# Kernel optimization log

Measured on AMD Instinct MI355X. Metric: run time of the kernel, lower is better.

## Reference

```python
import jax, jax.numpy as jnp
import numpy as np

N_NODES = 100000
N_EDGES = 1600000
IN_DIM, HID_DIM, LAT_DIM = 128, 128, 32


def gcn_conv(x, W, b, src, dst, ew, num_nodes):
    """PyG GCNConv with improved=True (self-loop fill value 2.0),
    symmetric normalization D^-1/2 (A + 2I) D^-1/2, then linear + bias."""
    loop = jnp.arange(num_nodes)
    src2 = jnp.concatenate([src, loop])
    dst2 = jnp.concatenate([dst, loop])
    ew2 = jnp.concatenate([ew, jnp.full((num_nodes,), 2.0, dtype=x.dtype)])
    # deg[i] = sum of incoming edge weights (incl. self loop weight 2)
    deg = jax.ops.segment_sum(ew2, dst2, num_segments=num_nodes)
    dinv = jnp.where(deg > 0, jax.lax.rsqrt(deg), 0.0)
    norm = dinv[src2] * ew2 * dinv[dst2]           # [E+N]
    h = x @ W                                      # linear first: [N, out]
    msg = h[src2] * norm[:, None]                  # gather + scale: [E+N, out]
    out = jax.ops.segment_sum(msg, dst2, num_segments=num_nodes)
    return out + b


def setup_inputs() -> dict:
    key = jax.random.key(0)
    ks = jax.random.split(key, 8)
    x = jax.random.normal(ks[0], (N_NODES, IN_DIM), dtype=jnp.float32)
    edge_index = jax.random.randint(ks[1], (2, N_EDGES), 0, N_NODES, dtype=jnp.int64)
    edge_weight = jnp.ones((N_EDGES,), dtype=jnp.float32)
    s = 1.0 / np.sqrt(IN_DIM)
    W1 = jax.random.normal(ks[2], (IN_DIM, HID_DIM), dtype=jnp.float32) * s
    b1 = jnp.zeros((HID_DIM,), dtype=jnp.float32)
    sh = 1.0 / np.sqrt(HID_DIM)
    Wm = jax.random.normal(ks[3], (HID_DIM, LAT_DIM), dtype=jnp.float32) * sh
    bm = jnp.zeros((LAT_DIM,), dtype=jnp.float32)
    Ws = jax.random.normal(ks[4], (HID_DIM, LAT_DIM), dtype=jnp.float32) * sh
    bs = jnp.zeros((LAT_DIM,), dtype=jnp.float32)
    return {"x": x, "edge_index": edge_index, "edge_weight": edge_weight,
            "W1": W1, "b1": b1, "Wm": Wm, "bm": bm, "Ws": Ws, "bs": bs}


def reference(x, edge_index, edge_weight, W1, b1, Wm, bm, Ws, bs):
    src, dst = edge_index[0], edge_index[1]
    n = x.shape[0]
    h = gcn_conv(x, W1, b1, src, dst, edge_weight, n)
    h = jax.nn.relu(h)
    z_mean = gcn_conv(h, Wm, bm, src, dst, edge_weight, n)
    z_logstd = gcn_conv(h, Ws, bs, src, dst, edge_weight, n)
    return (z_mean, z_logstd)
```

## Files before the change

### kernel.cpp

```cpp
#include <hip/hip_runtime.h>


#define DIM 128
#define LAT 32
#define SCAN_ELEMS 1024

typedef short bf16x8 __attribute__((ext_vector_type(8)));
typedef float f32x4 __attribute__((ext_vector_type(4)));

__device__ __forceinline__ unsigned short f2bf(float f) {
    unsigned u = __float_as_uint(f);
    return (unsigned short)((u + 0x7fffu + ((u >> 16) & 1u)) >> 16);
}
__device__ __forceinline__ unsigned packbf(float a, float b) {
    return (unsigned)f2bf(a) | ((unsigned)f2bf(b) << 16);
}
__device__ __forceinline__ float2 bfp2f(unsigned u) {
    float2 r;
    r.x = __uint_as_float(u << 16);
    r.y = __uint_as_float(u & 0xffff0000u);
    return r;
}

__global__ __launch_bounds__(256) void k_prep(const int* __restrict__ dst,
                                              int* __restrict__ cursor,
                                              unsigned short* __restrict__ rank, int E,
                                              const float* __restrict__ x,
                                              uint4* __restrict__ xb,
                                              const float* __restrict__ W1,
                                              const float* __restrict__ Wm,
                                              const float* __restrict__ Ws,
                                              unsigned short* __restrict__ w1t,
                                              unsigned short* __restrict__ wct,
                                              int RB, int XB) {
    const int b = blockIdx.x;
    if (b < RB) {
        int idx = b * 1024 + threadIdx.x * 4;
        if (idx + 3 < E) {
            int4 d4 = *reinterpret_cast<const int4*>(dst + idx);
            unsigned short r0 = (unsigned short)atomicAdd(&cursor[d4.x], 1);
            unsigned short r1 = (unsigned short)atomicAdd(&cursor[d4.y], 1);
            unsigned short r2 = (unsigned short)atomicAdd(&cursor[d4.z], 1);
            unsigned short r3 = (unsigned short)atomicAdd(&cursor[d4.w], 1);
            ushort4 r = {r0, r1, r2, r3};
            *reinterpret_cast<ushort4*>(rank + idx) = r;
        } else {
            for (int j = 0; j < 4 && idx + j < E; ++j)
                rank[idx + j] = (unsigned short)atomicAdd(&cursor[dst[idx + j]], 1);
        }
    } else if (b < RB + XB) {
        size_t i = ((size_t)(b - RB) * 256 + threadIdx.x) * 16;
        const float4* xin = reinterpret_cast<const float4*>(x + i);
        float4 v0 = xin[0], v1 = xin[1], v2 = xin[2], v3 = xin[3];
        uint4 o0, o1;
        o0.x = packbf(v0.x, v0.y); o0.y = packbf(v0.z, v0.w);
        o0.z = packbf(v1.x, v1.y); o0.w = packbf(v1.z, v1.w);
        o1.x = packbf(v2.x, v2.y); o1.y = packbf(v2.z, v2.w);
        o1.z = packbf(v3.x, v3.y); o1.w = packbf(v3.z, v3.w);
        xb[i / 8] = o0;
        xb[i / 8 + 1] = o1;
    } else {
        int i = (b - RB - XB) * 256 + threadIdx.x;
        if (i < DIM * DIM) {
            int c = i >> 7, k = i & 127;
            w1t[c * DIM + k] = f2bf(W1[k * DIM + c]);
        }
        i -= DIM * DIM;
        if (i >= 0 && i < 64 * DIM) {
            int c = i >> 7, k = i & 127;
            wct[c * DIM + k] = f2bf((c < LAT) ? Wm[k * LAT + c] : Ws[k * LAT + (c - LAT)]);
        }
    }
}

__global__ __launch_bounds__(256) void k_scan1(const int* __restrict__ counts,
                                               int* __restrict__ rowptr,
                                               int* __restrict__ bsums, int N) {
    __shared__ int sdata[256];
    const int t = threadIdx.x;
    const int base = blockIdx.x * SCAN_ELEMS + t * 4;
    int v[4];
#pragma unroll
    for (int j = 0; j < 4; ++j) {
        int idx = base + j;
        v[j] = (idx < N) ? counts[idx] : 0;
    }
    int tot = v[0] + v[1] + v[2] + v[3];
    sdata[t] = tot;
    __syncthreads();
    for (int off = 1; off < 256; off <<= 1) {
        int x = 0;
        if (t >= off) x = sdata[t - off];
        __syncthreads();
        if (t >= off) sdata[t] += x;
        __syncthreads();
    }
    int running = sdata[t] - tot;
#pragma unroll
    for (int j = 0; j < 4; ++j) {
        int idx = base + j;
        if (idx < N) rowptr[idx] = running;
        running += v[j];
    }
    if (t == 255) bsums[blockIdx.x] = sdata[255];
}

__global__ __launch_bounds__(256) void k_scanfix(int* __restrict__ rowptr,
                                                 const int* __restrict__ bsums,
                                                 int N, int E) {
    __shared__ int pfx;
    if (threadIdx.x == 0) {
        int s = 0;
        for (int j = 0; j < (int)blockIdx.x; ++j) s += bsums[j];
        pfx = s;
        if (blockIdx.x == 0) rowptr[N] = E;
    }
    __syncthreads();
    int s = pfx;
    int base = blockIdx.x * SCAN_ELEMS + threadIdx.x * 4;
#pragma unroll
    for (int j = 0; j < 4; ++j) {
        int idx = base + j;
        if (idx < N) rowptr[idx] += s;
    }
}

__global__ void k_place(const int* __restrict__ src, const int* __restrict__ dst,
                        const float* __restrict__ ew, const unsigned short* __restrict__ rank,
                        const int* __restrict__ rowptr, int2* __restrict__ csr, int E) {
    int e = blockIdx.x * blockDim.x + threadIdx.x;
    if (e < E)
        csr[rowptr[dst[e]] + rank[e]] = make_int2(src[e], __float_as_int(ew[e]));
}

__global__ void k_degseg(const int2* __restrict__ csr, const int* __restrict__ rowptr,
                         float* __restrict__ dinv, int N) {
    int i = blockIdx.x * blockDim.x + threadIdx.x;
    if (i >= N) return;
    float deg = 2.0f;
    int p = rowptr[i], end = rowptr[i + 1];
    for (; p < end; ++p) deg += __int_as_float(csr[p].y);
    dinv[i] = (deg > 0.0f) ? rsqrtf(deg) : 0.0f;
}

__global__ __launch_bounds__(256) void k_gather128(const int2* __restrict__ csr,
                                                   const int* __restrict__ rowptr,
                                                   const float* __restrict__ dinv,
                                                   const uint4* __restrict__ xb,
                                                   uint4* __restrict__ axb, int N) {
    int node = (blockIdx.x * 256 + threadIdx.x) >> 6;
    int lane = threadIdx.x & 63;
    if (node >= N) return;
    const int q = lane >> 4;
    const int l = lane & 15;
    float di = dinv[node];
    float acc[8];
#pragma unroll
    for (int j = 0; j < 8; ++j) acc[j] = 0.f;
    if (q == 0) {
        uint4 sv = xb[(size_t)node * 16 + l];
        float sl = 2.0f * di;
        float2 s0 = bfp2f(sv.x), s1 = bfp2f(sv.y), s2 = bfp2f(sv.z), s3 = bfp2f(sv.w);
        acc[0] = s0.x * sl; acc[1] = s0.y * sl;
        acc[2] = s1.x * sl; acc[3] = s1.y * sl;
        acc[4] = s2.x * sl; acc[5] = s2.y * sl;
        acc[6] = s3.x * sl; acc[7] = s3.y * sl;
    }
    int p = rowptr[node] + q;
    int end = rowptr[node + 1];
    for (; p + 12 < end; p += 16) {
        int2 e0 = csr[p], e1 = csr[p + 4], e2 = csr[p + 8], e3 = csr[p + 12];
        float n0 = __int_as_float(e0.y) * dinv[e0.x];
        float n1 = __int_as_float(e1.y) * dinv[e1.x];
        float n2 = __int_as_float(e2.y) * dinv[e2.x];
        float n3 = __int_as_float(e3.y) * dinv[e3.x];
        uint4 u0 = xb[(size_t)e0.x * 16 + l];
        uint4 u1 = xb[(size_t)e1.x * 16 + l];
        uint4 u2 = xb[(size_t)e2.x * 16 + l];
        uint4 u3 = xb[(size_t)e3.x * 16 + l];
        {
            float2 a0 = bfp2f(u0.x), a1 = bfp2f(u0.y), a2 = bfp2f(u0.z), a3 = bfp2f(u0.w);
            acc[0] = fmaf(a0.x, n0, acc[0]); acc[1] = fmaf(a0.y, n0, acc[1]);
            acc[2] = fmaf(a1.x, n0, acc[2]); acc[3] = fmaf(a1.y, n0, acc[3]);
            acc[4] = fmaf(a2.x, n0, acc[4]); acc[5] = fmaf(a2.y, n0, acc[5]);
            acc[6] = fmaf(a3.x, n0, acc[6]); acc[7] = fmaf(a3.y, n0, acc[7]);
        }
        {
            float2 a0 = bfp2f(u1.x), a1 = bfp2f(u1.y), a2 = bfp2f(u1.z), a3 = bfp2f(u1.w);
            acc[0] = fmaf(a0.x, n1, acc[0]); acc[1] = fmaf(a0.y, n1, acc[1]);
            acc[2] = fmaf(a1.x, n1, acc[2]); acc[3] = fmaf(a1.y, n1, acc[3]);
            acc[4] = fmaf(a2.x, n1, acc[4]); acc[5] = fmaf(a2.y, n1, acc[5]);
            acc[6] = fmaf(a3.x, n1, acc[6]); acc[7] = fmaf(a3.y, n1, acc[7]);
        }
        {
            float2 a0 = bfp2f(u2.x), a1 = bfp2f(u2.y), a2 = bfp2f(u2.z), a3 = bfp2f(u2.w);
            acc[0] = fmaf(a0.x, n2, acc[0]); acc[1] = fmaf(a0.y, n2, acc[1]);
            acc[2] = fmaf(a1.x, n2, acc[2]); acc[3] = fmaf(a1.y, n2, acc[3]);
            acc[4] = fmaf(a2.x, n2, acc[4]); acc[5] = fmaf(a2.y, n2, acc[5]);
            acc[6] = fmaf(a3.x, n2, acc[6]); acc[7] = fmaf(a3.y, n2, acc[7]);
        }
        {
            float2 a0 = bfp2f(u3.x), a1 = bfp2f(u3.y), a2 = bfp2f(u3.z), a3 = bfp2f(u3.w);
            acc[0] = fmaf(a0.x, n3, acc[0]); acc[1] = fmaf(a0.y, n3, acc[1]);
            acc[2] = fmaf(a1.x, n3, acc[2]); acc[3] = fmaf(a1.y, n3, acc[3]);
            acc[4] = fmaf(a2.x, n3, acc[4]); acc[5] = fmaf(a2.y, n3, acc[5]);
            acc[6] = fmaf(a3.x, n3, acc[6]); acc[7] = fmaf(a3.y, n3, acc[7]);
        }
    }
    for (; p < end; p += 4) {
        int2 e0 = csr[p];
        float n0 = __int_as_float(e0.y) * dinv[e0.x];
        uint4 u0 = xb[(size_t)e0.x * 16 + l];
        float2 a0 = bfp2f(u0.x), a1 = bfp2f(u0.y), a2 = bfp2f(u0.z), a3 = bfp2f(u0.w);
        acc[0] = fmaf(a0.x, n0, acc[0]); acc[1] = fmaf(a0.y, n0, acc[1]);
        acc[2] = fmaf(a1.x, n0, acc[2]); acc[3] = fmaf(a1.y, n0, acc[3]);
        acc[4] = fmaf(a2.x, n0, acc[4]); acc[5] = fmaf(a2.y, n0, acc[5]);
        acc[6] = fmaf(a3.x, n0, acc[6]); acc[7] = fmaf(a3.y, n0, acc[7]);
    }
#pragma unroll
    for (int j = 0; j < 8; ++j) {
        acc[j] += __shfl_xor(acc[j], 16);
        acc[j] += __shfl_xor(acc[j], 32);
    }
    if (q == 0) {
        uint4 o;
        o.x = packbf(acc[0] * di, acc[1] * di);
        o.y = packbf(acc[2] * di, acc[3] * di);
        o.z = packbf(acc[4] * di, acc[5] * di);
        o.w = packbf(acc[6] * di, acc[7] * di);
        axb[(size_t)node * 16 + l] = o;
    }
}

__global__ __launch_bounds__(256) void k_mfma_mlp(const unsigned short* __restrict__ axb,
                                                  const unsigned short* __restrict__ w1t,
                                                  const unsigned short* __restrict__ wct,
                                                  const float* __restrict__ b1,
                                                  unsigned short* __restrict__ hwb, int N) {
    __shared__ __align__(16) unsigned short hs[4][16][136];
    const int wave = threadIdx.x >> 6;
    const int lane = threadIdx.x & 63;
    const int lrow = lane & 15;
    const int lk = lane >> 4;
    const int R0 = blockIdx.x * 64 + wave * 16;
    const bool active = (R0 < N);

    if (active) {
        f32x4 acc[8];
#pragma unroll
        for (int t = 0; t < 8; ++t) acc[t] = (f32x4){0.f, 0.f, 0.f, 0.f};
        const unsigned short* arow = axb + (size_t)(R0 + lrow) * DIM + lk * 8;
#pragma unroll
        for (int kt = 0; kt < 4; ++kt) {
            bf16x8 a = *reinterpret_cast<const bf16x8*>(arow + kt * 32);
#pragma unroll
            for (int t = 0; t < 8; ++t) {
                bf16x8 b = *reinterpret_cast<const bf16x8*>(
                    w1t + (size_t)(t * 16 + lrow) * DIM + kt * 32 + lk * 8);
                acc[t] = __builtin_amdgcn_mfma_f32_16x16x32_bf16(a, b, acc[t], 0, 0, 0);
            }
        }
#pragma unroll
        for (int t = 0; t < 8; ++t) {
#pragma unroll
            for (int r = 0; r < 4; ++r) {
                int col = t * 16 + lrow;
                float v = acc[t][r] + b1[col];
                hs[wave][lk * 4 + r][col] = f2bf(v > 0.f ? v : 0.f);
            }
        }
    }
    __syncthreads();
    if (active) {
        f32x4 acc2[4];
#pragma unroll
        for (int t = 0; t < 4; ++t) acc2[t] = (f32x4){0.f, 0.f, 0.f, 0.f};
        const unsigned short* hrow = &hs[wave][lrow][0];
#pragma unroll
        for (int kt = 0; kt < 4; ++kt) {
            bf16x8 a = *reinterpret_cast<const bf16x8*>(hrow + kt * 32 + lk * 8);
#pragma unroll
            for (int t = 0; t < 4; ++t) {
                bf16x8 b = *reinterpret_cast<const bf16x8*>(
                    wct + (size_t)(t * 16 + lrow) * DIM + kt * 32 + lk * 8);
                acc2[t] = __builtin_amdgcn_mfma_f32_16x16x32_bf16(a, b, acc2[t], 0, 0, 0);
            }
        }
#pragma unroll
        for (int t = 0; t < 4; ++t)
#pragma unroll
            for (int r = 0; r < 4; ++r)
                hwb[(size_t)(R0 + lk * 4 + r) * 64 + t * 16 + lrow] = f2bf(acc2[t][r]);
    }
}

__global__ __launch_bounds__(256) void k_gather64(const int2* __restrict__ csr,
                                                  const int* __restrict__ rowptr,
                                                  const float* __restrict__ dinv,
                                                  const uint2* __restrict__ hwb,
                                                  const float* __restrict__ bm,
                                                  const float* __restrict__ bs,
                                                  float* __restrict__ outm,
                                                  float* __restrict__ outs, int N) {
    int node = (blockIdx.x * 256 + threadIdx.x) >> 6;
    int lane = threadIdx.x & 63;
    if (node >= N) return;
    const int q = lane >> 4;
    const int l = lane & 15;
    float di = dinv[node];
    float acc[4];
#pragma unroll
    for (int j = 0; j < 4; ++j) acc[j] = 0.f;
    if (q == 0) {
        uint2 sv = hwb[(size_t)node * 16 + l];
        float sl = 2.0f * di;
        float2 s0 = bfp2f(sv.x), s1 = bfp2f(sv.y);
        acc[0] = s0.x * sl; acc[1] = s0.y * sl;
        acc[2] = s1.x * sl; acc[3] = s1.y * sl;
    }
    int p = rowptr[node] + q;
    int end = rowptr[node + 1];
    for (; p + 12 < end; p += 16) {
        int2 e0 = csr[p], e1 = csr[p + 4], e2 = csr[p + 8], e3 = csr[p + 12];
        float n0 = __int_as_float(e0.y) * dinv[e0.x];
        float n1 = __int_as_float(e1.y) * dinv[e1.x];
        float n2 = __int_as_float(e2.y) * dinv[e2.x];
        float n3 = __int_as_float(e3.y) * dinv[e3.x];
        uint2 u0 = hwb[(size_t)e0.x * 16 + l];
        uint2 u1 = hwb[(size_t)e1.x * 16 + l];
        uint2 u2 = hwb[(size_t)e2.x * 16 + l];
        uint2 u3 = hwb[(size_t)e3.x * 16 + l];
        float2 a0 = bfp2f(u0.x), a1 = bfp2f(u0.y);
        acc[0] = fmaf(a0.x, n0, acc[0]); acc[1] = fmaf(a0.y, n0, acc[1]);
        acc[2] = fmaf(a1.x, n0, acc[2]); acc[3] = fmaf(a1.y, n0, acc[3]);
        float2 b0 = bfp2f(u1.x), b1 = bfp2f(u1.y);
        acc[0] = fmaf(b0.x, n1, acc[0]); acc[1] = fmaf(b0.y, n1, acc[1]);
        acc[2] = fmaf(b1.x, n1, acc[2]); acc[3] = fmaf(b1.y, n1, acc[3]);
        float2 c0 = bfp2f(u2.x), c1 = bfp2f(u2.y);
        acc[0] = fmaf(c0.x, n2, acc[0]); acc[1] = fmaf(c0.y, n2, acc[1]);
        acc[2] = fmaf(c1.x, n2, acc[2]); acc[3] = fmaf(c1.y, n2, acc[3]);
        float2 d0 = bfp2f(u3.x), d1 = bfp2f(u3.y);
        acc[0] = fmaf(d0.x, n3, acc[0]); acc[1] = fmaf(d0.y, n3, acc[1]);
        acc[2] = fmaf(d1.x, n3, acc[2]); acc[3] = fmaf(d1.y, n3, acc[3]);
    }
    for (; p < end; p += 4) {
        int2 e0 = csr[p];
        float n0 = __int_as_float(e0.y) * dinv[e0.x];
        uint2 u0 = hwb[(size_t)e0.x * 16 + l];
        float2 a0 = bfp2f(u0.x), a1 = bfp2f(u0.y);
        acc[0] = fmaf(a0.x, n0, acc[0]); acc[1] = fmaf(a0.y, n0, acc[1]);
        acc[2] = fmaf(a1.x, n0, acc[2]); acc[3] = fmaf(a1.y, n0, acc[3]);
    }
#pragma unroll
    for (int j = 0; j < 4; ++j) {
        acc[j] += __shfl_xor(acc[j], 16);
        acc[j] += __shfl_xor(acc[j], 32);
    }
    if (q == 0) {
        if (l < 8) {
            float4 bb = reinterpret_cast<const float4*>(bm)[l];
            float4 val;
            val.x = acc[0] * di + bb.x;
            val.y = acc[1] * di + bb.y;
            val.z = acc[2] * di + bb.z;
            val.w = acc[3] * di + bb.w;
            reinterpret_cast<float4*>(outm + (size_t)node * LAT)[l] = val;
        } else {
            float4 bb = reinterpret_cast<const float4*>(bs)[l - 8];
            float4 val;
            val.x = acc[0] * di + bb.x;
            val.y = acc[1] * di + bb.y;
            val.z = acc[2] * di + bb.z;
            val.w = acc[3] * di + bb.w;
            reinterpret_cast<float4*>(outs + (size_t)node * LAT)[l - 8] = val;
        }
    }
}

extern "C" void kernel_launch(void* const* d_in, const int* in_sizes, int n_in,
                              void* d_out, int out_size, void* d_ws, size_t ws_size,
                              hipStream_t stream) {
    const float* x  = (const float*)d_in[0];
    const int*   ei = (const int*)d_in[1];
    const float* ew = (const float*)d_in[2];
    const float* W1 = (const float*)d_in[3];
    const float* b1 = (const float*)d_in[4];
    const float* Wm = (const float*)d_in[5];
    const float* bm = (const float*)d_in[6];
    const float* Ws = (const float*)d_in[7];
    const float* bs = (const float*)d_in[8];

    const int N = in_sizes[0] / DIM;
    const int E = in_sizes[1] / 2;
    const int* src = ei;
    const int* dst = ei + E;

    char* w = (char*)d_ws;
    unsigned* xb  = (unsigned*)w;            w += (size_t)N * DIM * 2;
    unsigned* axb = (unsigned*)w;            w += (size_t)N * DIM * 2;
    unsigned short* hwb = (unsigned short*)w; w += (size_t)N * 64 * 2;
    float* dinv = (float*)w;                 w += (size_t)N * 4;
    int*   cursor = (int*)w;                 w += (size_t)N * 4;
    int*   rowptr = (int*)w;                 w += (size_t)(N + 1) * 4;
    unsigned short* rank = (unsigned short*)w; w += (size_t)E * 2;
    w = (char*)(((size_t)w + 255) & ~(size_t)255);
    int*   bsums  = (int*)w;                 w += 1024 * 4;
    unsigned short* w1t = (unsigned short*)w; w += DIM * DIM * 2;
    unsigned short* wct = (unsigned short*)w; w += 64 * DIM * 2;
    w = (char*)(((size_t)w + 255) & ~(size_t)255);
    int2*  csr    = (int2*)w;

    float* outm = (float*)d_out;
    float* outs = outm + (size_t)N * LAT;

    const int B = 256;
    const int NB = (N + SCAN_ELEMS - 1) / SCAN_ELEMS;
    const int RB = (E + 1023) / 1024;
    const int XB = (N * DIM / 16) / 256;
    const int WB = (DIM * DIM + 64 * DIM) / 256;

    hipMemsetAsync(cursor, 0, (size_t)N * 4, stream);
    k_prep<<<RB + XB + WB, B, 0, stream>>>(dst, cursor, rank, E, x, (uint4*)xb,
                                           W1, Wm, Ws, w1t, wct, RB, XB);

    k_scan1<<<NB, B, 0, stream>>>(cursor, rowptr, bsums, N);
    k_scanfix<<<NB, B, 0, stream>>>(rowptr, bsums, N, E);
    k_place<<<(E + B - 1) / B, B, 0, stream>>>(src, dst, ew, rank, rowptr, csr, E);
    k_degseg<<<(N + B - 1) / B, B, 0, stream>>>(csr, rowptr, dinv, N);

    k_gather128<<<(N + 3) / 4, B, 0, stream>>>(csr, rowptr, dinv, (const uint4*)xb, (uint4*)axb, N);

    k_mfma_mlp<<<(N + 63) / 64, B, 0, stream>>>((const unsigned short*)axb, w1t, wct, b1, hwb, N);

    k_gather64<<<(N + 3) / 4, B, 0, stream>>>(csr, rowptr, dinv, (const uint2*)hwb, bm, bs, outm, outs, N);
}
```

Before: 305.7 us.

## Build CSR via two-level bucket sort with shared-memory histograms

```diff
diff --git a/kernel.cpp b/kernel.cpp
--- a/kernel.cpp
+++ b/kernel.cpp
@@ -3,7 +3,8 @@
 
 #define DIM 128
 #define LAT 32
-#define SCAN_ELEMS 1024
+#define CHUNK 4096
+#define BSH 8
 
 typedef short bf16x8 __attribute__((ext_vector_type(8)));
 typedef float f32x4 __attribute__((ext_vector_type(4)));
@@ -22,9 +23,8 @@
     return r;
 }
 
-__global__ __launch_bounds__(256) void k_prep(const int* __restrict__ dst,
-                                              int* __restrict__ cursor,
-                                              unsigned short* __restrict__ rank, int E,
+__global__ __launch_bounds__(256) void k_hist(const int* __restrict__ dst, int E,
+                                              int* __restrict__ gh, int NCH, int NBK,
                                               const float* __restrict__ x,
                                               uint4* __restrict__ xb,
                                               const float* __restrict__ W1,
@@ -32,24 +32,19 @@
                                               const float* __restrict__ Ws,
                                               unsigned short* __restrict__ w1t,
                                               unsigned short* __restrict__ wct,
-                                              int RB, int XB) {
-    const int b = blockIdx.x;
-    if (b < RB) {
-        int idx = b * 1024 + threadIdx.x * 4;
-        if (idx + 3 < E) {
-            int4 d4 = *reinterpret_cast<const int4*>(dst + idx);
-            unsigned short r0 = (unsigned short)atomicAdd(&cursor[d4.x], 1);
-            unsigned short r1 = (unsigned short)atomicAdd(&cursor[d4.y], 1);
-            unsigned short r2 = (unsigned short)atomicAdd(&cursor[d4.z], 1);
-            unsigned short r3 = (unsigned short)atomicAdd(&cursor[d4.w], 1);
-            ushort4 r = {r0, r1, r2, r3};
-            *reinterpret_cast<ushort4*>(rank + idx) = r;
-        } else {
-            for (int j = 0; j < 4 && idx + j < E; ++j)
-                rank[idx + j] = (unsigned short)atomicAdd(&cursor[dst[idx + j]], 1);
-        }
-    } else if (b < RB + XB) {
-        size_t i = ((size_t)(b - RB) * 256 + threadIdx.x) * 16;
+                                              int XB) {
+    const int c = blockIdx.x;
+    if (c < NCH) {
+        __shared__ int h[512];
+        for (int b = threadIdx.x; b < NBK; b += 256) h[b] = 0;
+        __syncthreads();
+        int end = min(E, (c + 1) * CHUNK);
+        for (int e = c * CHUNK + threadIdx.x; e < end; e += 256)
+            atomicAdd(&h[dst[e] >> BSH], 1);
+        __syncthreads();
+        for (int b = threadIdx.x; b < NBK; b += 256) gh[b * NCH + c] = h[b];
+    } else if (c < NCH + XB) {
+        size_t i = ((size_t)(c - NCH) * 256 + threadIdx.x) * 16;
         const float4* xin = reinterpret_cast<const float4*>(x + i);
         float4 v0 = xin[0], v1 = xin[1], v2 = xin[2], v3 = xin[3];
         uint4 o0, o1;
@@ -60,87 +55,132 @@
         xb[i / 8] = o0;
         xb[i / 8 + 1] = o1;
     } else {
-        int i = (b - RB - XB) * 256 + threadIdx.x;
+        int i = (c - NCH - XB) * 256 + threadIdx.x;
         if (i < DIM * DIM) {
-            int c = i >> 7, k = i & 127;
-            w1t[c * DIM + k] = f2bf(W1[k * DIM + c]);
+            int cc = i >> 7, k = i & 127;
+            w1t[cc * DIM + k] = f2bf(W1[k * DIM + cc]);
         }
         i -= DIM * DIM;
         if (i >= 0 && i < 64 * DIM) {
-            int c = i >> 7, k = i & 127;
-            wct[c * DIM + k] = f2bf((c < LAT) ? Wm[k * LAT + c] : Ws[k * LAT + (c - LAT)]);
-        }
-    }
-}
-
-__global__ __launch_bounds__(256) void k_scan1(const int* __restrict__ counts,
+            int cc = i >> 7, k = i & 127;
+            wct[cc * DIM + k] = f2bf((cc < LAT) ? Wm[k * LAT + cc] : Ws[k * LAT + (cc - LAT)]);
+        }
+    }
+}
+
+__global__ __launch_bounds__(256) void k_btot(const int* __restrict__ gh, int NCH,
+                                              int* __restrict__ btot) {
+    __shared__ int sdata[256];
+    const int b = blockIdx.x;
+    int sum = 0;
+    for (int t = threadIdx.x; t < NCH; t += 256) sum += gh[b * NCH + t];
+    sdata[threadIdx.x] = sum;
+    __syncthreads();
+    for (int off = 128; off > 0; off >>= 1) {
+        if (threadIdx.x < off) sdata[threadIdx.x] += sdata[threadIdx.x + off];
+        __syncthreads();
+    }
+    if (threadIdx.x == 0) btot[b] = sdata[0];
+}
+
+__global__ __launch_bounds__(256) void k_rowscan(int* __restrict__ gh, int NCH, int NBK,
+                                                 const int* __restrict__ btot,
+                                                 int* __restrict__ bbase, int E) {
+    __shared__ int sdata[256];
+    __shared__ int basepfx;
+    const int b = blockIdx.x;
+    const int t = threadIdx.x;
+    if (t == 0) {
+        int s = 0;
+        for (int j = 0; j < b; ++j) s += btot[j];
+        basepfx = s;
+        bbase[b] = s;
+        if (b == NBK - 1) bbase[NBK] = s + btot[b];
+    }
+    __syncthreads();
+    int i0 = 2 * t, i1 = 2 * t + 1;
+    int v0 = (i0 < NCH) ? gh[b * NCH + i0] : 0;
+    int v1 = (i1 < NCH) ? gh[b * NCH + i1] : 0;
+    int tot = v0 + v1;
+    sdata[t] = tot;
+    __syncthreads();
+    for (int off = 1; off < 256; off <<= 1) {
+        int xv = 0;
+        if (t >= off) xv = sdata[t - off];
+        __syncthreads();
+        if (t >= off) sdata[t] += xv;
+        __syncthreads();
+    }
+    int pfx = basepfx + sdata[t] - tot;
+    if (i0 < NCH) gh[b * NCH + i0] = pfx;
+    if (i1 < NCH) gh[b * NCH + i1] = pfx + v0;
+}
+
+__global__ __launch_bounds__(256) void k_bucket(const int* __restrict__ src,
+                                                const int* __restrict__ dst,
+                                                const float* __restrict__ ew,
+                                                const int* __restrict__ gh, int NCH, int NBK,
+                                                int2* __restrict__ bkt, int E) {
+    __shared__ int cur[512];
+    const int c = blockIdx.x;
+    for (int b = threadIdx.x; b < NBK; b += 256) cur[b] = gh[b * NCH + c];
+    __syncthreads();
+    int end = min(E, (c + 1) * CHUNK);
+    for (int e = c * CHUNK + threadIdx.x; e < end; e += 256) {
+        int d = dst[e];
+        int b = d >> BSH;
+        int p = atomicAdd(&cur[b], 1);
+        bkt[p] = make_int2(src[e] | ((d & 255) << 17), __float_as_int(ew[e]));
+    }
+}
+
+__global__ __launch_bounds__(256) void k_build(const int2* __restrict__ bkt,
+                                               const int* __restrict__ bbase,
                                                int* __restrict__ rowptr,
-                                               int* __restrict__ bsums, int N) {
+                                               int2* __restrict__ csr,
+                                               float* __restrict__ dinv, int N, int E) {
+    __shared__ int cnt[256];
+    __shared__ int offs[256];
+    __shared__ int cnt2[256];
+    __shared__ float degf[256];
     __shared__ int sdata[256];
+    const int b = blockIdx.x;
     const int t = threadIdx.x;
-    const int base = blockIdx.x * SCAN_ELEMS + t * 4;
-    int v[4];
-#pragma unroll
-    for (int j = 0; j < 4; ++j) {
-        int idx = base + j;
-        v[j] = (idx < N) ? counts[idx] : 0;
-    }
-    int tot = v[0] + v[1] + v[2] + v[3];
-    sdata[t] = tot;
+    const int start = bbase[b], endb = bbase[b + 1];
+    cnt[t] = 0; cnt2[t] = 0; degf[t] = 0.f;
+    __syncthreads();
+    for (int idx = start + t; idx < endb; idx += 256) {
+        int2 rec = bkt[idx];
+        int dl = (rec.x >> 17) & 255;
+        atomicAdd(&cnt[dl], 1);
+        atomicAdd(&degf[dl], __int_as_float(rec.y));
+    }
+    __syncthreads();
+    int myc = cnt[t];
+    sdata[t] = myc;
     __syncthreads();
     for (int off = 1; off < 256; off <<= 1) {
-        int x = 0;
-        if (t >= off) x = sdata[t - off];
-        __syncthreads();
-        if (t >= off) sdata[t] += x;
-        __syncthreads();
-    }
-    int running = sdata[t] - tot;
-#pragma unroll
-    for (int j = 0; j < 4; ++j) {
-        int idx = base + j;
-        if (idx < N) rowptr[idx] = running;
-        running += v[j];
-    }
-    if (t == 255) bsums[blockIdx.x] = sdata[255];
-}
-
-__global__ __launch_bounds__(256) void k_scanfix(int* __restrict__ rowptr,
-                                                 const int* __restrict__ bsums,
-                                                 int N, int E) {
-    __shared__ int pfx;
-    if (threadIdx.x == 0) {
-        int s = 0;
-        for (int j = 0; j < (int)blockIdx.x; ++j) s += bsums[j];
-        pfx = s;
-        if (blockIdx.x == 0) rowptr[N] = E;
-    }
-    __syncthreads();
-    int s = pfx;
-    int base = blockIdx.x * SCAN_ELEMS + threadIdx.x * 4;
-#pragma unroll
-    for (int j = 0; j < 4; ++j) {
-        int idx = base + j;
-        if (idx < N) rowptr[idx] += s;
-    }
-}
-
-__global__ void k_place(const int* __restrict__ src, const int* __restrict__ dst,
-                        const float* __restrict__ ew, const unsigned short* __restrict__ rank,
-                        const int* __restrict__ rowptr, int2* __restrict__ csr, int E) {
-    int e = blockIdx.x * blockDim.x + threadIdx.x;
-    if (e < E)
-        csr[rowptr[dst[e]] + rank[e]] = make_int2(src[e], __float_as_int(ew[e]));
-}
-
-__global__ void k_degseg(const int2* __restrict__ csr, const int* __restrict__ rowptr,
-                         float* __restrict__ dinv, int N) {
-    int i = blockIdx.x * blockDim.x + threadIdx.x;
-    if (i >= N) return;
-    float deg = 2.0f;
-    int p = rowptr[i], end = rowptr[i + 1];
-    for (; p < end; ++p) deg += __int_as_float(csr[p].y);
-    dinv[i] = (deg > 0.0f) ? rsqrtf(deg) : 0.0f;
+        int xv = 0;
+        if (t >= off) xv = sdata[t - off];
+        __syncthreads();
+        if (t >= off) sdata[t] += xv;
+        __syncthreads();
+    }
+    offs[t] = sdata[t] - myc;
+    int node = (b << BSH) + t;
+    if (node < N) {
+        rowptr[node] = start + offs[t];
+        float deg = 2.0f + degf[t];
+        dinv[node] = (deg > 0.0f) ? rsqrtf(deg) : 0.0f;
+    }
+    if (b == 0 && t == 0) rowptr[N] = E;
+    __syncthreads();
+    for (int idx = start + t; idx < endb; idx += 256) {
+        int2 rec = bkt[idx];
+        int dl = (rec.x >> 17) & 255;
+        int r = atomicAdd(&cnt2[dl], 1);
+        csr[start + offs[dl] + r] = make_int2(rec.x & 0x1FFFF, rec.y);
+    }
 }
 
 __global__ __launch_bounds__(256) void k_gather128(const int2* __restrict__ csr,
@@ -395,42 +435,42 @@
     const int* src = ei;
     const int* dst = ei + E;
 
+    const int NCH = (E + CHUNK - 1) / CHUNK;
+    const int NBK = (N + 255) >> BSH;
+
     char* w = (char*)d_ws;
     unsigned* xb  = (unsigned*)w;            w += (size_t)N * DIM * 2;
     unsigned* axb = (unsigned*)w;            w += (size_t)N * DIM * 2;
     unsigned short* hwb = (unsigned short*)w; w += (size_t)N * 64 * 2;
     float* dinv = (float*)w;                 w += (size_t)N * 4;
-    int*   cursor = (int*)w;                 w += (size_t)N * 4;
     int*   rowptr = (int*)w;                 w += (size_t)(N + 1) * 4;
-    unsigned short* rank = (unsigned short*)w; w += (size_t)E * 2;
     w = (char*)(((size_t)w + 255) & ~(size_t)255);
-    int*   bsums  = (int*)w;                 w += 1024 * 4;
+    int*   gh    = (int*)w;                  w += (size_t)NBK * NCH * 4;
+    int*   btot  = (int*)w;                  w += (size_t)NBK * 4;
+    int*   bbase = (int*)w;                  w += (size_t)(NBK + 1) * 4;
+    w = (char*)(((size_t)w + 255) & ~(size_t)255);
     unsigned short* w1t = (unsigned short*)w; w += DIM * DIM * 2;
     unsigned short* wct = (unsigned short*)w; w += 64 * DIM * 2;
     w = (char*)(((size_t)w + 255) & ~(size_t)255);
-    int2*  csr    = (int2*)w;
+    int2*  bkt   = (int2*)w;                 w += (size_t)E * 8;
+    w = (char*)(((size_t)w + 255) & ~(size_t)255);
+    int2*  csr   = (int2*)w;
 
     float* outm = (float*)d_out;
     float* outs = outm + (size_t)N * LAT;
 
     const int B = 256;
-    const int NB = (N + SCAN_ELEMS - 1) / SCAN_ELEMS;
-    const int RB = (E + 1023) / 1024;
     const int XB = (N * DIM / 16) / 256;
     const int WB = (DIM * DIM + 64 * DIM) / 256;
 
-    hipMemsetAsync(cursor, 0, (size_t)N * 4, stream);
-    k_prep<<<RB + XB + WB, B, 0, stream>>>(dst, cursor, rank, E, x, (uint4*)xb,
-                                           W1, Wm, Ws, w1t, wct, RB, XB);
-
-    k_scan1<<<NB, B, 0, stream>>>(cursor, rowptr, bsums, N);
-    k_scanfix<<<NB, B, 0, stream>>>(rowptr, bsums, N, E);
-    k_place<<<(E + B - 1) / B, B, 0, stream>>>(src, dst, ew, rank, rowptr, csr, E);
-    k_degseg<<<(N + B - 1) / B, B, 0, stream>>>(csr, rowptr, dinv, N);
+    k_hist<<<NCH + XB + WB, B, 0, stream>>>(dst, E, gh, NCH, NBK, x, (uint4*)xb,
+                                            W1, Wm, Ws, w1t, wct, XB);
+    k_btot<<<NBK, B, 0, stream>>>(gh, NCH, btot);
+    k_rowscan<<<NBK, B, 0, stream>>>(gh, NCH, NBK, btot, bbase, E);
+    k_bucket<<<NCH, B, 0, stream>>>(src, dst, ew, gh, NCH, NBK, bkt, E);
+    k_build<<<NBK, B, 0, stream>>>(bkt, bbase, rowptr, csr, dinv, N, E);
 
     k_gather128<<<(N + 3) / 4, B, 0, stream>>>(csr, rowptr, dinv, (const uint4*)xb, (uint4*)axb, N);
-
     k_mfma_mlp<<<(N + 63) / 64, B, 0, stream>>>((const unsigned short*)axb, w1t, wct, b1, hwb, N);
-
     k_gather64<<<(N + 3) / 4, B, 0, stream>>>(csr, rowptr, dinv, (const uint2*)hwb, bm, bs, outm, outs, N);
 }
```

After: 255.2 us (median of 3 runs). 16.5% less time.
